# Optimization experiments

Measured on AMD Instinct MI355X. Metric: run time of the kernel, lower is better.

The kernel has to match this reference:

```python
import jax, jax.numpy as jnp
import numpy as np

N_HEAD = 16
N_EMBD = 1024
BLOCK = 2048
B, T = 4, 2048


def setup_inputs() -> dict:
    key = jax.random.key(0)
    ks = jax.random.split(key, 5)
    s = 0.02
    return {
        "x": jax.random.normal(ks[0], (B, T, N_EMBD), dtype=jnp.float32),
        "qkv_w": jax.random.normal(ks[1], (3 * N_EMBD, N_EMBD), dtype=jnp.float32) * s,
        "qkv_b": jnp.zeros((3 * N_EMBD,), dtype=jnp.float32),
        "proj_w": jax.random.normal(ks[2], (N_EMBD, N_EMBD), dtype=jnp.float32) * s,
        "proj_b": jnp.zeros((N_EMBD,), dtype=jnp.float32),
    }


def reference(x, qkv_w, qkv_b, proj_w, proj_b):
    Bx, Tx, C = x.shape
    hd = C // N_HEAD
    qkv = x @ qkv_w.T + qkv_b  # [B,T,3C]
    q, k, v = jnp.split(qkv, 3, axis=-1)
    # [B,T,C] -> [B,H,T,hd]
    def heads(t):
        return t.reshape(Bx, Tx, N_HEAD, hd).transpose(0, 2, 1, 3)
    q, k, v = heads(q), heads(k), heads(v)
    scores = jnp.einsum("bhqd,bhkd->bhqk", q, k) / jnp.sqrt(jnp.float32(hd))
    causal = jnp.tril(jnp.ones((Tx, Tx), dtype=bool))
    scores = jnp.where(causal[None, None, :, :], scores, -jnp.inf)
    attn = jax.nn.softmax(scores, axis=-1)
    out = jnp.einsum("bhqk,bhkd->bhqd", attn, v)
    out = out.transpose(0, 2, 1, 3).reshape(Bx, Tx, C)
    return out @ proj_w.T + proj_b
```

## Files before the change

kernel.cpp:

```cpp
#include <hip/hip_runtime.h>
#include <stdint.h>
#include <math.h>

#define DEVI __device__ __forceinline__

typedef __attribute__((ext_vector_type(8))) short bf16x8;
typedef __attribute__((ext_vector_type(4))) float f32x4;

DEVI unsigned short f2bf(float f) {
  union { float f; unsigned u; } v; v.f = f;
  unsigned u = v.u;
  u += 0x7fffu + ((u >> 16) & 1u);
  return (unsigned short)(u >> 16);
}

DEVI unsigned cvt_pk_bf16(float a, float b) {
  unsigned r;
  asm("v_cvt_pk_bf16_f32 %0, %1, %2" : "=v"(r) : "v"(a), "v"(b));
  return r;
}

DEVI f32x4 mfma16(bf16x8 a, bf16x8 b, f32x4 c) {
  return __builtin_amdgcn_mfma_f32_16x16x32_bf16(a, b, c, 0, 0, 0);
}

DEVI void gld16(const unsigned short* g, unsigned short* l) {
  __builtin_amdgcn_global_load_lds(
      (const __attribute__((address_space(1))) unsigned int*)(uintptr_t)g,
      (__attribute__((address_space(3))) unsigned int*)(unsigned int)(uintptr_t)l,
      16, 0, 0);
}

#define VMCNT(n) asm volatile("s_waitcnt vmcnt(" #n ")" ::: "memory")
#define BAR()                              \
  do {                                     \
    __builtin_amdgcn_s_barrier();          \
    __builtin_amdgcn_sched_barrier(0);     \
  } while (0)

template <int N> DEVI void vmcntc() {
  static_assert(N >= 0 && N <= 8, "");
  if constexpr (N == 0) VMCNT(0);
  else if constexpr (N == 2) VMCNT(2);
  else if constexpr (N == 3) VMCNT(3);
  else if constexpr (N == 4) VMCNT(4);
}

__global__ __launch_bounds__(256) void cvt3_kernel(
    const float* __restrict__ a, unsigned short* __restrict__ oa,
    const float* __restrict__ b, unsigned short* __restrict__ ob,
    const float* __restrict__ c, unsigned short* __restrict__ oc) {
  int bid = blockIdx.x;
  const float* in; unsigned short* out; int i;
  if (bid < 8192)       { in = a; out = oa; i = bid; }
  else if (bid < 11264) { in = b; out = ob; i = bid - 8192; }
  else                  { in = c; out = oc; i = bid - 11264; }
  int idx = (i * 256 + (int)threadIdx.x) * 4;
  float4 v = *(const float4*)(in + idx);
  unsigned lo = f2bf(v.x) | ((unsigned)f2bf(v.y) << 16);
  unsigned hi = f2bf(v.z) | ((unsigned)f2bf(v.w) << 16);
  uint2 o; o.x = lo; o.y = hi;
  *(uint2*)(out + idx) = o;
}

template <int MODE, int NTA, int NTB>
__global__ __launch_bounds__(512, 2) void gemm8(
    const unsigned short* __restrict__ A, const unsigned short* __restrict__ Bw,
    const float* __restrict__ bias, float* __restrict__ Cf,
    unsigned short* __restrict__ Qo, unsigned short* __restrict__ Ko,
    unsigned short* __restrict__ Vo, int M, int N, int K, int nbx) {
  constexpr int NTT = NTA + NTB;
  constexpr int WTN = NTT * 16;
  constexpr int BN = 4 * WTN;
  constexpr int B_USH = BN * 64;
  constexpr int BUFS = 16384 + B_USH;
  extern __shared__ unsigned short lds[];
  const int tid = threadIdx.x;
  const int lane = tid & 63;
  const int w = tid >> 6;
  const int wm = w >> 2, wn = w & 3;
  const int lr = lane & 15, lq = lane >> 4;

  const int cpx = gridDim.x >> 3;
  const int swz = (blockIdx.x & 7) * cpx + (blockIdx.x >> 3);
  const int bx = swz % nbx, by = swz / nbx;
  const int m0 = by * 256, n0 = bx * BN;

  const int sr = lane >> 3;
  const int sc = ((lane & 7) ^ sr) << 3;
  const unsigned short* pa = A + (size_t)(m0 + sr) * K + sc;
  const unsigned short* pb = Bw + (size_t)(n0 + sr) * K + sc;

  const int bs0 = (lq ^ (lr & 7)) << 3;
  const int bs1 = ((lq + 4) ^ (lr & 7)) << 3;

  f32x4 acc[8][NTT] = {};

  auto sA = [&](int buf, int kt, int c) {
    gld16(pa + (size_t)(c << 3) * K + kt, lds + buf * BUFS + (c << 9));
  };
  auto sB = [&](int buf, int kt, int c) {
    gld16(pb + (size_t)(c << 3) * K + kt, lds + buf * BUFS + 16384 + (c << 9));
  };
  auto sAa = [&](int buf, int kt) { sA(buf, kt, w); sA(buf, kt, 16 + w); };
  auto sAb = [&](int buf, int kt) { sA(buf, kt, 8 + w); sA(buf, kt, 24 + w); };
  auto sBa = [&](int buf, int kt) {
#pragma unroll
    for (int k2 = 0; k2 < NTA; ++k2)
      sB(buf, kt, (w & 3) * NTT * 2 + (w >> 2) * NTA + k2);
  };
  auto sBb = [&](int buf, int kt) {
#pragma unroll
    for (int k2 = 0; k2 < NTB; ++k2)
      sB(buf, kt, (w & 3) * NTT * 2 + NTA * 2 + (w >> 2) * NTB + k2);
  };

#define LDA(A_, mh)                                                          \
  _Pragma("unroll") for (int i = 0; i < 4; ++i) {                            \
    int ar = wm * 128 + (mh) * 64 + i * 16 + lr;                             \
    A_[i][0] = *(const bf16x8*)(As_ + ar * 64 + bs0);                        \
    A_[i][1] = *(const bf16x8*)(As_ + ar * 64 + bs1);                        \
  }
#define LDB(B_, CNT, ntb)                                                    \
  _Pragma("unroll") for (int j = 0; j < (CNT); ++j) {                        \
    int br = wn * WTN + ((ntb) + j) * 16 + lr;                               \
    B_[j][0] = *(const bf16x8*)(Bs_ + br * 64 + bs0);                        \
    B_[j][1] = *(const bf16x8*)(Bs_ + br * 64 + bs1);                        \
  }
#define MM(A_, B_, mh, CNT, ntb)                                             \
  __builtin_amdgcn_s_setprio(1);                                             \
  _Pragma("unroll") for (int i = 0; i < 4; ++i)                              \
    _Pragma("unroll") for (int j = 0; j < (CNT); ++j) {                      \
      acc[(mh) * 4 + i][(ntb) + j] =                                         \
          mfma16(A_[i][0], B_[j][0], acc[(mh) * 4 + i][(ntb) + j]);          \
      acc[(mh) * 4 + i][(ntb) + j] =                                         \
          mfma16(A_[i][1], B_[j][1], acc[(mh) * 4 + i][(ntb) + j]);          \
    }                                                                        \
  __builtin_amdgcn_s_setprio(0);

  sAa(0, 0); sBa(0, 0); sBb(0, 0); sAb(0, 0);
  vmcntc<NTB + 2>();
  BAR();

  const int NT = K >> 6;
  for (int t = 0; t < NT - 1; ++t) {
    const int buf = t & 1, nb = buf ^ 1;
    const int kt = (t + 1) << 6;
    const unsigned short* As_ = lds + buf * BUFS;
    const unsigned short* Bs_ = As_ + 16384;
    bf16x8 af[4][2], baf[NTA][2], bbf[NTB][2];
    sAa(nb, kt);
    LDA(af, 0); LDB(baf, NTA, 0);
    MM(af, baf, 0, NTA, 0);
    vmcntc<4>(); BAR();
    sBa(nb, kt);
    LDB(bbf, NTB, NTA);
    MM(af, bbf, 0, NTB, NTA);
    vmcntc<NTA + 2>(); BAR();
    sBb(nb, kt);
    LDA(af, 1);
    MM(af, bbf, 1, NTB, NTA);
    sAb(nb, kt);
    MM(af, baf, 1, NTA, 0);
    vmcntc<NTB + 2>(); BAR();
  }
  {
    const int buf = (NT - 1) & 1;
    const unsigned short* As_ = lds + buf * BUFS;
    const unsigned short* Bs_ = As_ + 16384;
    bf16x8 af[4][2], baf[NTA][2], bbf[NTB][2];
    LDA(af, 0); LDB(baf, NTA, 0);
    MM(af, baf, 0, NTA, 0);
    vmcntc<2>(); BAR();
    LDB(bbf, NTB, NTA);
    MM(af, bbf, 0, NTB, NTA);
    vmcntc<0>(); BAR();
    LDA(af, 1);
    MM(af, bbf, 1, NTB, NTA);
    MM(af, baf, 1, NTA, 0);
  }
#undef LDA
#undef LDB
#undef MM

#pragma unroll
  for (int mt = 0; mt < 8; ++mt) {
#pragma unroll
    for (int nt = 0; nt < NTT; ++nt) {
      int n_g = n0 + wn * WTN + nt * 16 + lr;
      float bv = bias[n_g];
      if (MODE == 1) {
#pragma unroll
        for (int r = 0; r < 4; ++r) {
          int m_g = m0 + wm * 128 + mt * 16 + lq * 4 + r;
          Cf[(size_t)m_g * N + n_g] = acc[mt][nt][r] + bv;
        }
      } else {
        int which = n_g >> 10;
        int rem = n_g & 1023;
        int h = rem >> 6, d = rem & 63;
        int m_base = m0 + wm * 128 + mt * 16 + lq * 4;
        int b = m_base >> 11, tt = m_base & 2047;
        if (which == 2) {
          uint2 pv;
          pv.x = cvt_pk_bf16(acc[mt][nt][0] + bv, acc[mt][nt][1] + bv);
          pv.y = cvt_pk_bf16(acc[mt][nt][2] + bv, acc[mt][nt][3] + bv);
          *(uint2*)(Vo + (((size_t)(b * 16 + h) * 64 + d) * 2048 + tt)) = pv;
        } else {
          unsigned short* p = (which == 0) ? Qo : Ko;
#pragma unroll
          for (int r = 0; r < 4; ++r) {
            size_t idx = (((size_t)(b * 16 + h) * 2048) + tt + r) * 64 + d;
            p[idx] = f2bf(acc[mt][nt][r] + bv);
          }
        }
      }
    }
  }
}

__global__ __launch_bounds__(512, 2) void attn_kernel(
    const unsigned short* __restrict__ Q, const unsigned short* __restrict__ K,
    const unsigned short* __restrict__ V, unsigned short* __restrict__ Y) {
  constexpr int T = 2048, HD = 64, H = 16;
  __shared__ unsigned short Kt[2][64 * 72];
  __shared__ unsigned short Vt[2][64 * 72];
  __shared__ unsigned short Pt[8][16 * 72];

  const int tid = threadIdx.x;
  const int lane = tid & 63;
  const int w = tid >> 6;
  const int lr = lane & 15, lq = lane >> 4;
  const int pair = blockIdx.x;
  const int h = blockIdx.y;
  const int b = blockIdx.z;
  const size_t bh = (size_t)(b * H + h) * T * HD;
  const float SC = 0.125f * 1.44269504089f;

  const int krow = tid >> 3, kcb = (tid & 7) << 3;

  float4 kr, vr;
  auto load_tile = [&](int jt) {
    const int c0 = jt * 64;
    kr = *(const float4*)(K + bh + (size_t)(c0 + krow) * HD + kcb);
    vr = *(const float4*)(V + bh + (size_t)krow * T + c0 + kcb);
  };
  auto stage = [&](int buf) {
    *(float4*)(&Kt[buf][krow * 72 + kcb]) = kr;
    *(float4*)(&Vt[buf][krow * 72 + kcb]) = vr;
  };

  load_tile(0);

  for (int phase = 0; phase < 2; ++phase) {
    const int qt = phase ? (7 - pair) : pair;
    const int q0 = qt * 256;
    const int nkv = 4 * (qt + 1);
    const int qw = q0 + w * 32;

    bf16x8 qf[2][2];
#pragma unroll
    for (int qs = 0; qs < 2; ++qs)
#pragma unroll
      for (int kb = 0; kb < 2; ++kb)
        qf[qs][kb] = *(const bf16x8*)(Q + bh + (size_t)(qw + qs * 16 + lr) * HD +
                                      kb * 32 + lq * 8);

    f32x4 o[2][4] = {};
    float mi[2] = {-INFINITY, -INFINITY}, li[2] = {0.f, 0.f};

    stage(0);
    load_tile(1);
    __syncthreads();

    for (int jt = 0; jt < nkv; ++jt) {
      const int c0 = jt * 64;
      const int buf = jt & 1;

      if (c0 <= qw + 31) {
        f32x4 s[2][4];
        __builtin_amdgcn_s_setprio(1);
#pragma unroll
        for (int nt = 0; nt < 4; ++nt) {
          bf16x8 kf0 = *(const bf16x8*)(&Kt[buf][(nt * 16 + lr) * 72 + lq * 8]);
          bf16x8 kf1 = *(const bf16x8*)(&Kt[buf][(nt * 16 + lr) * 72 + 32 + lq * 8]);
#pragma unroll
          for (int qs = 0; qs < 2; ++qs) {
            f32x4 z = {};
            z = mfma16(kf0, qf[qs][0], z);
            s[qs][nt] = mfma16(kf1, qf[qs][1], z);
          }
        }
        __builtin_amdgcn_s_setprio(0);
        if (c0 + 63 > qw) {
#pragma unroll
          for (int qs = 0; qs < 2; ++qs) {
            int qg = qw + qs * 16 + lr;
#pragma unroll
            for (int nt = 0; nt < 4; ++nt)
#pragma unroll
              for (int r = 0; r < 4; ++r) {
                int kvg = c0 + nt * 16 + lq * 4 + r;
                if (kvg > qg) s[qs][nt][r] = -INFINITY;
              }
          }
        }
        float mxs[2];
#pragma unroll
        for (int qs = 0; qs < 2; ++qs) {
          float mx = -INFINITY;
#pragma unroll
          for (int nt = 0; nt < 4; ++nt)
            mx = fmaxf(mx, fmaxf(fmaxf(s[qs][nt][0], s[qs][nt][1]),
                                 fmaxf(s[qs][nt][2], s[qs][nt][3])));
          mx = fmaxf(mx, __shfl_xor(mx, 16));
          mx = fmaxf(mx, __shfl_xor(mx, 32));
          mxs[qs] = mx * SC;
        }
        if (!__all((mxs[0] <= mi[0] + 8.f) && (mxs[1] <= mi[1] + 8.f))) {
#pragma unroll
          for (int qs = 0; qs < 2; ++qs) {
            float mnew = fmaxf(mi[qs], mxs[qs]);
            float alpha = __builtin_amdgcn_exp2f(mi[qs] - mnew);
            mi[qs] = mnew;
            li[qs] *= alpha;
#pragma unroll
            for (int nt = 0; nt < 4; ++nt)
#pragma unroll
              for (int r = 0; r < 4; ++r) o[qs][nt][r] *= alpha;
          }
        }
        bf16x8 pf[2][2];
#pragma unroll
        for (int qs = 0; qs < 2; ++qs) {
          float rs = 0.f;
#pragma unroll
          for (int nt = 0; nt < 4; ++nt) {
            float p0 = __builtin_amdgcn_exp2f(fmaf(s[qs][nt][0], SC, -mi[qs]));
            float p1 = __builtin_amdgcn_exp2f(fmaf(s[qs][nt][1], SC, -mi[qs]));
            float p2 = __builtin_amdgcn_exp2f(fmaf(s[qs][nt][2], SC, -mi[qs]));
            float p3 = __builtin_amdgcn_exp2f(fmaf(s[qs][nt][3], SC, -mi[qs]));
            rs += (p0 + p1) + (p2 + p3);
            uint2 pk;
            pk.x = cvt_pk_bf16(p0, p1);
            pk.y = cvt_pk_bf16(p2, p3);
            *(uint2*)(&Pt[w][lr * 72 + nt * 16 + lq * 4]) = pk;
          }
          li[qs] += rs;
#pragma unroll
          for (int kb = 0; kb < 2; ++kb)
            pf[qs][kb] = *(const bf16x8*)(&Pt[w][lr * 72 + kb * 32 + lq * 8]);
        }
        __builtin_amdgcn_s_setprio(1);
#pragma unroll
        for (int nt = 0; nt < 4; ++nt) {
          bf16x8 vf0 = *(const bf16x8*)(&Vt[buf][(nt * 16 + lr) * 72 + lq * 8]);
          bf16x8 vf1 = *(const bf16x8*)(&Vt[buf][(nt * 16 + lr) * 72 + 32 + lq * 8]);
#pragma unroll
          for (int qs = 0; qs < 2; ++qs) {
            o[qs][nt] = mfma16(vf0, pf[qs][0], o[qs][nt]);
            o[qs][nt] = mfma16(vf1, pf[qs][1], o[qs][nt]);
          }
        }
        __builtin_amdgcn_s_setprio(0);
      }

      if (jt + 1 < nkv) {
        stage(buf ^ 1);
        if (jt + 2 < nkv) load_tile(jt + 2);
        else if (phase == 0) load_tile(0);
        __syncthreads();
      }
    }

#pragma unroll
    for (int qs = 0; qs < 2; ++qs) {
      float l = li[qs];
      l += __shfl_xor(l, 16);
      l += __shfl_xor(l, 32);
      float inv = 1.f / l;
      int t_g = qw + qs * 16 + lr;
#pragma unroll
      for (int nt = 0; nt < 4; ++nt) {
        uint2 yv;
        yv.x = cvt_pk_bf16(o[qs][nt][0] * inv, o[qs][nt][1] * inv);
        yv.y = cvt_pk_bf16(o[qs][nt][2] * inv, o[qs][nt][3] * inv);
        *(uint2*)(Y + ((size_t)(b * T + t_g)) * 1024 + h * 64 + nt * 16 + lq * 4) = yv;
      }
    }
  }
}

extern "C" void kernel_launch(void* const* d_in, const int* in_sizes, int n_in,
                              void* d_out, int out_size, void* d_ws, size_t ws_size,
                              hipStream_t stream) {
  const float* x = (const float*)d_in[0];
  const float* qkv_w = (const float*)d_in[1];
  const float* qkv_b = (const float*)d_in[2];
  const float* proj_w = (const float*)d_in[3];
  const float* proj_b = (const float*)d_in[4];
  float* out = (float*)d_out;

  unsigned short* ws = (unsigned short*)d_ws;
  unsigned short* xb = ws;
  unsigned short* wqkv = xb + 8388608;
  unsigned short* wproj = wqkv + 3145728;
  unsigned short* Qb = wproj + 1048576;
  unsigned short* Kb = Qb + 8388608;
  unsigned short* Vb = Kb + 8388608;
  unsigned short* Yb = Vb + 8388608;

  auto* g0 = gemm8<0, 2, 1>;
  auto* g1 = gemm8<1, 1, 1>;
  static bool attr_set = false;
  if (!attr_set) {
    (void)hipFuncSetAttribute((const void*)g0,
                              hipFuncAttributeMaxDynamicSharedMemorySize, 114688);
    (void)hipFuncSetAttribute((const void*)g1,
                              hipFuncAttributeMaxDynamicSharedMemorySize, 98304);
    attr_set = true;
  }

  cvt3_kernel<<<12288, 256, 0, stream>>>(x, xb, qkv_w, wqkv, proj_w, wproj);

  gemm8<0, 2, 1><<<dim3(512), 512, 114688, stream>>>(xb, wqkv, qkv_b, nullptr, Qb,
                                                     Kb, Vb, 8192, 3072, 1024, 16);
  attn_kernel<<<dim3(4, 16, 4), 512, 0, stream>>>(Qb, Kb, Vb, Yb);
  gemm8<1, 1, 1><<<dim3(256), 512, 98304, stream>>>(Yb, wproj, proj_b, out, nullptr,
                                                    nullptr, nullptr, 8192, 1024,
                                                    1024, 8);
}
```

Measured before the change: 239.2 us.

## Halve per-block query tile in attention to double grid and occupancy

The attention kernel now has each warp handle 16 query rows instead of 32, so a block covers 128 queries per phase. The grid grows from 256 to 512 blocks with a remapped linear block index, and launch bounds ask for 4 blocks per SM. Balanced causal pairing is kept across tiles and half-tiles. This is meant to fill the GPU better and hide latency through higher occupancy. The cost is that K/V tiles are loaded from global memory and staged in shared memory twice as often per query, and each loaded tile feeds fewer MFMAs.

```diff
diff --git a/kernel.cpp b/kernel.cpp
--- a/kernel.cpp
+++ b/kernel.cpp
@@ -219,7 +219,7 @@
   }
 }
 
-__global__ __launch_bounds__(512, 2) void attn_kernel(
+__global__ __launch_bounds__(512, 4) void attn_kernel(
     const unsigned short* __restrict__ Q, const unsigned short* __restrict__ K,
     const unsigned short* __restrict__ V, unsigned short* __restrict__ Y) {
   constexpr int T = 2048, HD = 64, H = 16;
@@ -231,9 +231,11 @@
   const int lane = tid & 63;
   const int w = tid >> 6;
   const int lr = lane & 15, lq = lane >> 4;
-  const int pair = blockIdx.x;
-  const int h = blockIdx.y;
-  const int b = blockIdx.z;
+  const int lin = blockIdx.x;
+  const int h = (lin >> 2) & 15;
+  const int b = lin & 3;
+  const int p = (lin >> 7) & 3;
+  const int hf = (lin >> 6) & 1;
   const size_t bh = (size_t)(b * H + h) * T * HD;
   const float SC = 0.125f * 1.44269504089f;
 
@@ -253,21 +255,19 @@
   load_tile(0);
 
   for (int phase = 0; phase < 2; ++phase) {
-    const int qt = phase ? (7 - pair) : pair;
-    const int q0 = qt * 256;
-    const int nkv = 4 * (qt + 1);
-    const int qw = q0 + w * 32;
-
-    bf16x8 qf[2][2];
-#pragma unroll
-    for (int qs = 0; qs < 2; ++qs)
-#pragma unroll
-      for (int kb = 0; kb < 2; ++kb)
-        qf[qs][kb] = *(const bf16x8*)(Q + bh + (size_t)(qw + qs * 16 + lr) * HD +
-                                      kb * 32 + lq * 8);
-
-    f32x4 o[2][4] = {};
-    float mi[2] = {-INFINITY, -INFINITY}, li[2] = {0.f, 0.f};
+    const int qt = phase ? (7 - p) : p;
+    const int hh = phase ? (1 - hf) : hf;
+    const int q0 = qt * 256 + hh * 128;
+    const int nkv = 4 * qt + 2 * hh + 2;
+    const int qw = q0 + w * 16;
+
+    bf16x8 qf[2];
+#pragma unroll
+    for (int kb = 0; kb < 2; ++kb)
+      qf[kb] = *(const bf16x8*)(Q + bh + (size_t)(qw + lr) * HD + kb * 32 + lq * 8);
+
+    f32x4 o[4] = {};
+    float mi = -INFINITY, li = 0.f;
 
     stage(0);
     load_tile(1);
@@ -277,90 +277,71 @@
       const int c0 = jt * 64;
       const int buf = jt & 1;
 
-      if (c0 <= qw + 31) {
-        f32x4 s[2][4];
+      if (c0 <= qw + 15) {
+        f32x4 s[4];
         __builtin_amdgcn_s_setprio(1);
 #pragma unroll
         for (int nt = 0; nt < 4; ++nt) {
           bf16x8 kf0 = *(const bf16x8*)(&Kt[buf][(nt * 16 + lr) * 72 + lq * 8]);
           bf16x8 kf1 = *(const bf16x8*)(&Kt[buf][(nt * 16 + lr) * 72 + 32 + lq * 8]);
-#pragma unroll
-          for (int qs = 0; qs < 2; ++qs) {
-            f32x4 z = {};
-            z = mfma16(kf0, qf[qs][0], z);
-            s[qs][nt] = mfma16(kf1, qf[qs][1], z);
-          }
+          f32x4 z = {};
+          z = mfma16(kf0, qf[0], z);
+          s[nt] = mfma16(kf1, qf[1], z);
         }
         __builtin_amdgcn_s_setprio(0);
         if (c0 + 63 > qw) {
-#pragma unroll
-          for (int qs = 0; qs < 2; ++qs) {
-            int qg = qw + qs * 16 + lr;
-#pragma unroll
-            for (int nt = 0; nt < 4; ++nt)
-#pragma unroll
-              for (int r = 0; r < 4; ++r) {
-                int kvg = c0 + nt * 16 + lq * 4 + r;
-                if (kvg > qg) s[qs][nt][r] = -INFINITY;
-              }
-          }
-        }
-        float mxs[2];
-#pragma unroll
-        for (int qs = 0; qs < 2; ++qs) {
-          float mx = -INFINITY;
+          int qg = qw + lr;
 #pragma unroll
           for (int nt = 0; nt < 4; ++nt)
-            mx = fmaxf(mx, fmaxf(fmaxf(s[qs][nt][0], s[qs][nt][1]),
-                                 fmaxf(s[qs][nt][2], s[qs][nt][3])));
-          mx = fmaxf(mx, __shfl_xor(mx, 16));
-          mx = fmaxf(mx, __shfl_xor(mx, 32));
-          mxs[qs] = mx * SC;
-        }
-        if (!__all((mxs[0] <= mi[0] + 8.f) && (mxs[1] <= mi[1] + 8.f))) {
-#pragma unroll
-          for (int qs = 0; qs < 2; ++qs) {
-            float mnew = fmaxf(mi[qs], mxs[qs]);
-            float alpha = __builtin_amdgcn_exp2f(mi[qs] - mnew);
-            mi[qs] = mnew;
-            li[qs] *= alpha;
-#pragma unroll
-            for (int nt = 0; nt < 4; ++nt)
-#pragma unroll
-              for (int r = 0; r < 4; ++r) o[qs][nt][r] *= alpha;
-          }
-        }
-        bf16x8 pf[2][2];
-#pragma unroll
-        for (int qs = 0; qs < 2; ++qs) {
-          float rs = 0.f;
-#pragma unroll
-          for (int nt = 0; nt < 4; ++nt) {
-            float p0 = __builtin_amdgcn_exp2f(fmaf(s[qs][nt][0], SC, -mi[qs]));
-            float p1 = __builtin_amdgcn_exp2f(fmaf(s[qs][nt][1], SC, -mi[qs]));
-            float p2 = __builtin_amdgcn_exp2f(fmaf(s[qs][nt][2], SC, -mi[qs]));
-            float p3 = __builtin_amdgcn_exp2f(fmaf(s[qs][nt][3], SC, -mi[qs]));
-            rs += (p0 + p1) + (p2 + p3);
-            uint2 pk;
-            pk.x = cvt_pk_bf16(p0, p1);
-            pk.y = cvt_pk_bf16(p2, p3);
-            *(uint2*)(&Pt[w][lr * 72 + nt * 16 + lq * 4]) = pk;
-          }
-          li[qs] += rs;
-#pragma unroll
-          for (int kb = 0; kb < 2; ++kb)
-            pf[qs][kb] = *(const bf16x8*)(&Pt[w][lr * 72 + kb * 32 + lq * 8]);
-        }
+#pragma unroll
+            for (int r = 0; r < 4; ++r) {
+              int kvg = c0 + nt * 16 + lq * 4 + r;
+              if (kvg > qg) s[nt][r] = -INFINITY;
+            }
+        }
+        float mx = -INFINITY;
+#pragma unroll
+        for (int nt = 0; nt < 4; ++nt)
+          mx = fmaxf(mx, fmaxf(fmaxf(s[nt][0], s[nt][1]),
+                               fmaxf(s[nt][2], s[nt][3])));
+        mx = fmaxf(mx, __shfl_xor(mx, 16));
+        mx = fmaxf(mx, __shfl_xor(mx, 32));
+        float mxs = mx * SC;
+        if (!__all(mxs <= mi + 8.f)) {
+          float mnew = fmaxf(mi, mxs);
+          float alpha = __builtin_amdgcn_exp2f(mi - mnew);
+          mi = mnew;
+          li *= alpha;
+#pragma unroll
+          for (int nt = 0; nt < 4; ++nt)
+#pragma unroll
+            for (int r = 0; r < 4; ++r) o[nt][r] *= alpha;
+        }
+        float rs = 0.f;
+#pragma unroll
+        for (int nt = 0; nt < 4; ++nt) {
+          float p0 = __builtin_amdgcn_exp2f(fmaf(s[nt][0], SC, -mi));
+          float p1 = __builtin_amdgcn_exp2f(fmaf(s[nt][1], SC, -mi));
+          float p2 = __builtin_amdgcn_exp2f(fmaf(s[nt][2], SC, -mi));
+          float p3 = __builtin_amdgcn_exp2f(fmaf(s[nt][3], SC, -mi));
+          rs += (p0 + p1) + (p2 + p3);
+          uint2 pk;
+          pk.x = cvt_pk_bf16(p0, p1);
+          pk.y = cvt_pk_bf16(p2, p3);
+          *(uint2*)(&Pt[w][lr * 72 + nt * 16 + lq * 4]) = pk;
+        }
+        li += rs;
+        bf16x8 pf[2];
+#pragma unroll
+        for (int kb = 0; kb < 2; ++kb)
+          pf[kb] = *(const bf16x8*)(&Pt[w][lr * 72 + kb * 32 + lq * 8]);
         __builtin_amdgcn_s_setprio(1);
 #pragma unroll
         for (int nt = 0; nt < 4; ++nt) {
           bf16x8 vf0 = *(const bf16x8*)(&Vt[buf][(nt * 16 + lr) * 72 + lq * 8]);
           bf16x8 vf1 = *(const bf16x8*)(&Vt[buf][(nt * 16 + lr) * 72 + 32 + lq * 8]);
-#pragma unroll
-          for (int qs = 0; qs < 2; ++qs) {
-            o[qs][nt] = mfma16(vf0, pf[qs][0], o[qs][nt]);
-            o[qs][nt] = mfma16(vf1, pf[qs][1], o[qs][nt]);
-          }
+          o[nt] = mfma16(vf0, pf[0], o[nt]);
+          o[nt] = mfma16(vf1, pf[1], o[nt]);
         }
         __builtin_amdgcn_s_setprio(0);
       }
@@ -373,18 +354,17 @@
       }
     }
 
-#pragma unroll
-    for (int qs = 0; qs < 2; ++qs) {
-      float l = li[qs];
+    {
+      float l = li;
       l += __shfl_xor(l, 16);
       l += __shfl_xor(l, 32);
       float inv = 1.f / l;
-      int t_g = qw + qs * 16 + lr;
+      int t_g = qw + lr;
 #pragma unroll
       for (int nt = 0; nt < 4; ++nt) {
         uint2 yv;
-        yv.x = cvt_pk_bf16(o[qs][nt][0] * inv, o[qs][nt][1] * inv);
-        yv.y = cvt_pk_bf16(o[qs][nt][2] * inv, o[qs][nt][3] * inv);
+        yv.x = cvt_pk_bf16(o[nt][0] * inv, o[nt][1] * inv);
+        yv.y = cvt_pk_bf16(o[nt][2] * inv, o[nt][3] * inv);
         *(uint2*)(Y + ((size_t)(b * T + t_g)) * 1024 + h * 64 + nt * 16 + lq * 4) = yv;
       }
     }
@@ -425,7 +405,7 @@
 
   gemm8<0, 2, 1><<<dim3(512), 512, 114688, stream>>>(xb, wqkv, qkv_b, nullptr, Qb,
                                                      Kb, Vb, 8192, 3072, 1024, 16);
-  attn_kernel<<<dim3(4, 16, 4), 512, 0, stream>>>(Qb, Kb, Vb, Yb);
+  attn_kernel<<<dim3(512), 512, 0, stream>>>(Qb, Kb, Vb, Yb);
   gemm8<1, 1, 1><<<dim3(256), 512, 98304, stream>>>(Yb, wproj, proj_b, out, nullptr,
                                                     nullptr, nullptr, 8192, 1024,
                                                     1024, 8);
```

New measurement: 246.8 us. +3.2%, slower.
